# Performance work log

Measured on AMD Instinct MI355X. Metric: run time of the kernel, lower is better.

The kernel has to match this reference:

```python
import jax, jax.numpy as jnp
import numpy as np
from jax import lax

# --- constants derived from init args ---
TAU = 0.1
CNSTS = (1.0, 10.0)
EPSILON = CNSTS[0] / TAU          # 10.0
LAMBDAA = CNSTS[0] * CNSTS[1] / TAU  # 100.0
ALPHA = 0.5
SIGMA = 2.0
ITER_NUM = 5
IN_CHANNELS = 3
M = max(4 * int(2 * SIGMA) + 1, 5)  # 17


def gauss_kernel():
    # 2D normalized Gaussian, shape [C, 1, M, M] for depthwise conv (OIHW with groups=C)
    xx = jnp.arange(M, dtype=jnp.float32) - (M - 1.0) / 2.0
    d2 = xx[:, None] ** 2 + xx[None, :] ** 2
    w = jnp.exp(-d2 / (2.0 * SIGMA ** 2))
    w = w / w.sum()
    return jnp.broadcast_to(w[None, None], (IN_CHANNELS, 1, M, M))


def depthwise_conv(x, w):
    # x: [B, C, H, W], w: [C, 1, M, M]; SAME padding (M odd, pad = M//2)
    return lax.conv_general_dilated(
        x, w, window_strides=(1, 1), padding='SAME',
        dimension_numbers=('NCHW', 'OIHW', 'NCHW'),
        feature_group_count=IN_CHANNELS)


def setup_inputs() -> dict:
    key = jax.random.key(0)
    k1, k2 = jax.random.split(key)
    x = jax.random.uniform(k1, (8, 3, 512, 512), dtype=jnp.float32)
    c = jax.random.normal(k2, (8, 3, 512, 512), dtype=jnp.float32)
    return {'x': x, 'c': c}


def reference(x, c):
    w = gauss_kernel()
    b = jax.nn.sigmoid(10.0 * c)          # getb(c)
    lam_b = LAMBDAA * b
    u = jax.nn.sigmoid(-(lam_b * depthwise_conv(1.0 - 2.0 * x, w)) / EPSILON)
    for _ in range(max(abs(ITER_NUM), 1)):
        uu = (u - x) / TAU + lam_b * depthwise_conv(1.0 - 2.0 * u, w)
        uu = jax.nn.sigmoid(-uu / EPSILON)
        u = (1.0 - ALPHA) * u + ALPHA * uu
    return u
```

## Files before the change

### kernel.cpp

```cpp
#include <hip/hip_runtime.h>
#include <hip/hip_fp16.h>
#include <math.h>


#define TR   32
#define TC   64
#define HR   48
#define RAD  8
#define HW   512
#define NIMG 24
#define NPIX ((size_t)HW * HW * NIMG)

__device__ __constant__ const float GWc[17] = {
    6.6916e-05f, 4.3635e-04f, 2.2159612e-03f, 8.7643070e-03f,
    2.6995958e-02f, 6.4759932e-02f, 1.2098751e-01f, 1.7603572e-01f,
    1.9947466e-01f,
    1.7603572e-01f, 1.2098751e-01f, 6.4759932e-02f, 2.6995958e-02f,
    8.7643070e-03f, 2.2159612e-03f, 4.3635e-04f, 6.6916e-05f
};

struct alignas(16) H8 { __half2 a, b, c, d; };

__device__ __forceinline__ float inv1pexp(float z) {
    return __builtin_amdgcn_rcpf(1.0f + __expf(z));
}

template<int MODE>
__global__ __launch_bounds__(256, 8) void sig_step(
    const float* __restrict__ xg, const float* __restrict__ cgl,
    const __half* __restrict__ uin, __half2* __restrict__ xl,
    void* __restrict__ uout)
{
    __shared__ __half sTmp[HR * TC];

    const int t    = threadIdx.x;
    const int img  = blockIdx.z;
    const int row0 = blockIdx.y * TR;
    const int col0 = blockIdx.x * TC;
    const size_t ibase = (size_t)img * HW * HW;

#pragma unroll
    for (int i = 0; i < 2; ++i) {
        int q = t + i * 256;
        if (q < HR * 8) {
            int r  = q >> 3;
            int ci = q & 7;
            int gr = row0 + r - RAD;
            float w[24];
#pragma unroll
            for (int j = 0; j < 24; ++j) w[j] = 0.5f;
            if (gr >= 0 && gr < HW) {
                int gc0 = col0 + ci * 8 - RAD;
                if constexpr (MODE == 0) {
                    const float* xb = xg + ibase + (size_t)gr * HW;
#pragma unroll
                    for (int j = 0; j < 6; ++j) {
                        int s = gc0 + 4 * j;
                        if (s >= 0 && s < HW) {
                            float4 v = *reinterpret_cast<const float4*>(&xb[s]);
                            w[4*j+0] = v.x; w[4*j+1] = v.y;
                            w[4*j+2] = v.z; w[4*j+3] = v.w;
                        }
                    }
                } else {
                    const __half* ub = uin + ibase + (size_t)gr * HW;
#pragma unroll
                    for (int j = 0; j < 3; ++j) {
                        int s = gc0 + 8 * j;
                        if (s >= 0 && s < HW) {
                            H8 v = *reinterpret_cast<const H8*>(&ub[s]);
                            float2 f0 = __half22float2(v.a);
                            float2 f1 = __half22float2(v.b);
                            float2 f2 = __half22float2(v.c);
                            float2 f3 = __half22float2(v.d);
                            w[8*j+0] = f0.x; w[8*j+1] = f0.y;
                            w[8*j+2] = f1.x; w[8*j+3] = f1.y;
                            w[8*j+4] = f2.x; w[8*j+5] = f2.y;
                            w[8*j+6] = f3.x; w[8*j+7] = f3.y;
                        }
                    }
                }
            }
            float a[8];
#pragma unroll
            for (int j = 0; j < 8; ++j) {
                float acc = 0.f;
#pragma unroll
                for (int k = 0; k < 17; ++k) acc += GWc[k] * w[j + k];
                a[j] = acc;
            }
            H8 o;
            o.a = __floats2half2_rn(a[0], a[1]);
            o.b = __floats2half2_rn(a[2], a[3]);
            o.c = __floats2half2_rn(a[4], a[5]);
            o.d = __floats2half2_rn(a[6], a[7]);
            *reinterpret_cast<H8*>(&sTmp[r * TC + ci * 8]) = o;
        }
    }
    __syncthreads();

    const int cc = t & 63;
    const int rg = t >> 6;
    const size_t pbase = ibase + (size_t)(row0 + rg * 8) * HW + (col0 + cc);

    float win[24];
#pragma unroll
    for (int j = 0; j < 24; ++j)
        win[j] = __half2float(sTmp[(rg * 8 + j) * TC + cc]);

#pragma unroll
    for (int m = 0; m < 8; ++m) {
        float v = 0.f;
#pragma unroll
        for (int k = 0; k < 17; ++k) v += GWc[k] * win[m + k];
        float f = 1.f - 2.f * v;

        size_t gidx = pbase + (size_t)m * HW;
        if constexpr (MODE == 0) {
            float xv  = xg[gidx];
            float lam = 100.f * inv1pexp(-10.f * cgl[gidx]);
            xl[gidx] = __floats2half2_rn(xv, lam);
            ((__half*)uout)[gidx] = __float2half(inv1pexp(lam * f * 0.1f));
        } else {
            float2 p = __half22float2(xl[gidx]);
            float uprev = __half2float(uin[gidx]);
            float tt = (uprev - p.x) * 10.f + p.y * f;
            float uu = inv1pexp(tt * 0.1f);
            float res = 0.5f * (uprev + uu);
            if constexpr (MODE == 2) ((float*)uout)[gidx] = res;
            else                     ((__half*)uout)[gidx] = __float2half(res);
        }
    }
}

extern "C" void kernel_launch(void* const* d_in, const int* in_sizes, int n_in,
                              void* d_out, int out_size, void* d_ws, size_t ws_size,
                              hipStream_t stream) {
    const float* x = (const float*)d_in[0];
    const float* c = (const float*)d_in[1];

    __half* u0 = (__half*)d_ws;
    __half* u1 = u0 + NPIX;
    __half2* xl = (ws_size >= NPIX * 8)
        ? (__half2*)((char*)d_ws + NPIX * 4)
        : (__half2*)d_out;

    dim3 grid(HW / TC, HW / TR, NIMG);
    dim3 block(256);
    sig_step<0><<<grid, block, 0, stream>>>(x, c, nullptr, xl, u0);
    sig_step<1><<<grid, block, 0, stream>>>(x, c, u0, xl, u1);
    sig_step<1><<<grid, block, 0, stream>>>(x, c, u1, xl, u0);
    sig_step<1><<<grid, block, 0, stream>>>(x, c, u0, xl, u1);
    sig_step<1><<<grid, block, 0, stream>>>(x, c, u1, xl, u0);
    sig_step<2><<<grid, block, 0, stream>>>(x, c, u0, xl, d_out);
}
```

Measured before the change: 116.4 us.

## Use packed fp16 dot2 for horizontal Gaussian pass with 16 outputs per thread

Rewrites the horizontal 17-tap blur to keep inputs packed as half2 and accumulate with v_dot2 (fp16 pairs into fp32), using alignbit to form the odd-shifted pairs. Each of 192 threads now produces 16 outputs instead of 8, which roughly halves the instruction count for the horizontal pass and drops the separate unpack-to-float work. Launch bounds are lowered to 6 waves because register pressure rises. The Gaussian weights are rounded to fp16, and in mode 0 the fp32 x values are also rounded to fp16 before the blur, which adds some precision loss.

```diff
diff --git a/kernel.cpp b/kernel.cpp
--- a/kernel.cpp
+++ b/kernel.cpp
@@ -11,22 +11,49 @@
 #define NIMG 24
 #define NPIX ((size_t)HW * HW * NIMG)
 
+typedef _Float16 h2 __attribute__((ext_vector_type(2)));
+typedef unsigned int uint;
+
+#define G0  6.6916e-05f
+#define G1  4.3635e-04f
+#define G2  2.2159612e-03f
+#define G3  8.7643070e-03f
+#define G4  2.6995958e-02f
+#define G5  6.4759932e-02f
+#define G6  1.2098751e-01f
+#define G7  1.7603572e-01f
+#define G8  1.9947466e-01f
 __device__ __constant__ const float GWc[17] = {
-    6.6916e-05f, 4.3635e-04f, 2.2159612e-03f, 8.7643070e-03f,
-    2.6995958e-02f, 6.4759932e-02f, 1.2098751e-01f, 1.7603572e-01f,
-    1.9947466e-01f,
-    1.7603572e-01f, 1.2098751e-01f, 6.4759932e-02f, 2.6995958e-02f,
-    8.7643070e-03f, 2.2159612e-03f, 4.3635e-04f, 6.6916e-05f
+    G0,G1,G2,G3,G4,G5,G6,G7,G8,G7,G6,G5,G4,G3,G2,G1,G0
 };
-
-struct alignas(16) H8 { __half2 a, b, c, d; };
 
 __device__ __forceinline__ float inv1pexp(float z) {
     return __builtin_amdgcn_rcpf(1.0f + __expf(z));
 }
 
+__device__ __forceinline__ float fdot2f(uint a, h2 b, float c) {
+#if __has_builtin(__builtin_amdgcn_fdot2)
+    return __builtin_amdgcn_fdot2(__builtin_bit_cast(h2, a), b, c, false);
+#else
+    h2 av = __builtin_bit_cast(h2, a);
+    return (float)av.x * (float)b.x + (float)av.y * (float)b.y + c;
+#endif
+}
+__device__ __forceinline__ float lo16f(uint v) {
+    __half h = __ushort_as_half((unsigned short)(v & 0xffffu));
+    return __half2float(h);
+}
+__device__ __forceinline__ float hi16f(uint v) {
+    __half h = __ushort_as_half((unsigned short)(v >> 16));
+    return __half2float(h);
+}
+__device__ __forceinline__ h2 gpair(int i) {
+    const float G[16] = { G0,G1,G2,G3,G4,G5,G6,G7,G8,G7,G6,G5,G4,G3,G2,G1 };
+    h2 r; r.x = (_Float16)G[2*i]; r.y = (_Float16)G[2*i+1]; return r;
+}
+
 template<int MODE>
-__global__ __launch_bounds__(256, 8) void sig_step(
+__global__ __launch_bounds__(256, 6) void sig_step(
     const float* __restrict__ xg, const float* __restrict__ cgl,
     const __half* __restrict__ uin, __half2* __restrict__ xl,
     void* __restrict__ uout)
@@ -39,63 +66,65 @@
     const int col0 = blockIdx.x * TC;
     const size_t ibase = (size_t)img * HW * HW;
 
+    if (t < 192) {
+        const int r   = t >> 2;
+        const int ci2 = t & 3;
+        const int gr  = row0 + r - RAD;
+        const int gc0 = col0 + ci2 * 16 - RAD;
+
+        uint wv[16];
 #pragma unroll
-    for (int i = 0; i < 2; ++i) {
-        int q = t + i * 256;
-        if (q < HR * 8) {
-            int r  = q >> 3;
-            int ci = q & 7;
-            int gr = row0 + r - RAD;
-            float w[24];
+        for (int i = 0; i < 16; ++i) wv[i] = 0x38003800u;
+        if (gr >= 0 && gr < HW) {
+            if constexpr (MODE == 0) {
 #pragma unroll
-            for (int j = 0; j < 24; ++j) w[j] = 0.5f;
-            if (gr >= 0 && gr < HW) {
-                int gc0 = col0 + ci * 8 - RAD;
-                if constexpr (MODE == 0) {
-                    const float* xb = xg + ibase + (size_t)gr * HW;
+                for (int k = 0; k < 4; ++k) {
+                    int s = gc0 + 8 * k;
+                    if (s >= 0 && s < HW) {
+                        const float* xb = xg + ibase + (size_t)gr * HW + s;
+                        float4 va = *reinterpret_cast<const float4*>(xb);
+                        float4 vb = *reinterpret_cast<const float4*>(xb + 4);
+                        wv[4*k+0] = __builtin_bit_cast(uint, __floats2half2_rn(va.x, va.y));
+                        wv[4*k+1] = __builtin_bit_cast(uint, __floats2half2_rn(va.z, va.w));
+                        wv[4*k+2] = __builtin_bit_cast(uint, __floats2half2_rn(vb.x, vb.y));
+                        wv[4*k+3] = __builtin_bit_cast(uint, __floats2half2_rn(vb.z, vb.w));
+                    }
+                }
+            } else {
 #pragma unroll
-                    for (int j = 0; j < 6; ++j) {
-                        int s = gc0 + 4 * j;
-                        if (s >= 0 && s < HW) {
-                            float4 v = *reinterpret_cast<const float4*>(&xb[s]);
-                            w[4*j+0] = v.x; w[4*j+1] = v.y;
-                            w[4*j+2] = v.z; w[4*j+3] = v.w;
-                        }
-                    }
-                } else {
-                    const __half* ub = uin + ibase + (size_t)gr * HW;
-#pragma unroll
-                    for (int j = 0; j < 3; ++j) {
-                        int s = gc0 + 8 * j;
-                        if (s >= 0 && s < HW) {
-                            H8 v = *reinterpret_cast<const H8*>(&ub[s]);
-                            float2 f0 = __half22float2(v.a);
-                            float2 f1 = __half22float2(v.b);
-                            float2 f2 = __half22float2(v.c);
-                            float2 f3 = __half22float2(v.d);
-                            w[8*j+0] = f0.x; w[8*j+1] = f0.y;
-                            w[8*j+2] = f1.x; w[8*j+3] = f1.y;
-                            w[8*j+4] = f2.x; w[8*j+5] = f2.y;
-                            w[8*j+6] = f3.x; w[8*j+7] = f3.y;
-                        }
+                for (int k = 0; k < 4; ++k) {
+                    int s = gc0 + 8 * k;
+                    if (s >= 0 && s < HW) {
+                        uint4 v = *reinterpret_cast<const uint4*>(
+                                      uin + ibase + (size_t)gr * HW + s);
+                        wv[4*k+0] = v.x; wv[4*k+1] = v.y;
+                        wv[4*k+2] = v.z; wv[4*k+3] = v.w;
                     }
                 }
             }
-            float a[8];
+        }
+        uint wo[15];
 #pragma unroll
-            for (int j = 0; j < 8; ++j) {
-                float acc = 0.f;
+        for (int i = 0; i < 15; ++i)
+            wo[i] = __builtin_amdgcn_alignbit(wv[i + 1], wv[i], 16);
+
+        uint ow[8];
 #pragma unroll
-                for (int k = 0; k < 17; ++k) acc += GWc[k] * w[j + k];
-                a[j] = acc;
+        for (int jp = 0; jp < 8; ++jp) {
+            float a0 = 0.f, a1 = 0.f;
+#pragma unroll
+            for (int i = 0; i < 8; ++i) {
+                h2 g = gpair(i);
+                a0 = fdot2f(wv[jp + i], g, a0);
+                a1 = fdot2f(wo[jp + i], g, a1);
             }
-            H8 o;
-            o.a = __floats2half2_rn(a[0], a[1]);
-            o.b = __floats2half2_rn(a[2], a[3]);
-            o.c = __floats2half2_rn(a[4], a[5]);
-            o.d = __floats2half2_rn(a[6], a[7]);
-            *reinterpret_cast<H8*>(&sTmp[r * TC + ci * 8]) = o;
+            a0 = fmaf(G0, lo16f(wv[jp + 8]), a0);
+            a1 = fmaf(G0, hi16f(wv[jp + 8]), a1);
+            ow[jp] = __builtin_bit_cast(uint, __floats2half2_rn(a0, a1));
         }
+        uint4* orow = reinterpret_cast<uint4*>(&sTmp[r * TC + ci2 * 16]);
+        orow[0] = make_uint4(ow[0], ow[1], ow[2], ow[3]);
+        orow[1] = make_uint4(ow[4], ow[5], ow[6], ow[7]);
     }
     __syncthreads();
 
```

Result: faster. 102.2 us (-12.2%).
